# Performance work log

Hardware: AMD Instinct MI355X
Metric: run time of the kernel (lower is better)

Reference implementation:

```python
import jax, jax.numpy as jnp
import numpy as np

NEG_SLOPE = 0.2
CHUNK = 64  # target-node chunk size to bound the [B,c,N,H,D] intermediate


def layer_norm(x, g, b, eps=1e-5):
    mu = jnp.mean(x, axis=-1, keepdims=True)
    var = jnp.mean((x - mu) ** 2, axis=-1, keepdims=True)
    return (x - mu) / jnp.sqrt(var + eps) * g + b


def gatv2_dense(x, Wl, bl, Wr, br, att, bias):
    """GATv2 (PyG semantics, concat=True) on a fully-connected graph with self-loops.
    x: [B,N,Fin]; att: [H,D]. Returns [B,N,H*D].
    e_ij = att_h . leaky_relu(xl_j + xr_i); softmax over sources j; out_i = sum_j a_ij xl_j.
    """
    B, N, _ = x.shape
    H, D = att.shape
    xl = (x @ Wl + bl).reshape(B, N, H, D)  # source-side (lin_l)
    xr = (x @ Wr + br).reshape(B, N, H, D)  # target-side (lin_r)
    nc = N // CHUNK
    xr_ch = jnp.moveaxis(xr.reshape(B, nc, CHUNK, H, D), 1, 0)  # [nc,B,c,H,D]

    @jax.checkpoint
    def per_chunk(xr_c):  # xr_c: [B,c,H,D]
        z = jax.nn.leaky_relu(xr_c[:, :, None] + xl[:, None], NEG_SLOPE)  # [B,c,N,H,D]
        e = jnp.einsum('bcjhd,hd->bcjh', z, att)
        a = jax.nn.softmax(e, axis=2)  # softmax over sources j
        return jnp.einsum('bcjh,bjhd->bchd', a, xl)

    out = jax.lax.map(per_chunk, xr_ch)  # [nc,B,c,H,D]
    return jnp.moveaxis(out, 0, 1).reshape(B, N, H * D) + bias


def setup_inputs() -> dict:
    key = jax.random.key(0)
    ks = jax.random.split(key, 12)
    B, N, Fin, Hd, H, Do = 4, 2048, 32, 32, 4, 32
    f32 = jnp.float32

    def glorot(k, shape, fan_in):
        return jax.random.normal(k, shape, f32) * (1.0 / np.sqrt(fan_in))

    return {
        'x': jax.random.normal(ks[0], (B, N, Fin), f32),
        'embedding': jax.random.normal(ks[1], (N, Hd), f32),
        # layer 1: in=Fin, heads=H, head dim=Hd
        'Wl1': glorot(ks[2], (Fin, H * Hd), Fin), 'bl1': jnp.zeros((H * Hd,), f32),
        'Wr1': glorot(ks[3], (Fin, H * Hd), Fin), 'br1': jnp.zeros((H * Hd,), f32),
        'att1': glorot(ks[4], (H, Hd), Hd), 'bias1': jnp.zeros((H * Hd,), f32),
        'ln1_g': jnp.ones((H * Hd,), f32), 'ln1_b': jnp.zeros((H * Hd,), f32),
        # layer 2: in=H*Hd, heads=H, head dim=Do
        'Wl2': glorot(ks[5], (H * Hd, H * Do), H * Hd), 'bl2': jnp.zeros((H * Do,), f32),
        'Wr2': glorot(ks[6], (H * Hd, H * Do), H * Hd), 'br2': jnp.zeros((H * Do,), f32),
        'att2': glorot(ks[7], (H, Do), Do), 'bias2': jnp.zeros((H * Do,), f32),
        'ln2_g': jnp.ones((H * Do,), f32), 'ln2_b': jnp.zeros((H * Do,), f32),
    }


def reference(x, embedding, Wl1, bl1, Wr1, br1, att1, bias1, ln1_g, ln1_b,
              Wl2, bl2, Wr2, br2, att2, bias2, ln2_g, ln2_b):
    # AdaptiveAdjacency: cosine-similarity gram matrix. Its values are generically
    # all nonzero, so adj[b].nonzero() yields a fully-connected edge list including
    # self-loops; only the connectivity (dense) is consumed downstream.
    ne = embedding / jnp.linalg.norm(embedding, axis=1, keepdims=True)
    adj = ne @ ne.T  # [N,N]; connectivity only (dense), values unused by GATv2
    del adj

    h = layer_norm(gatv2_dense(x, Wl1, bl1, Wr1, br1, att1, bias1), ln1_g, ln1_b)
    h = jax.nn.relu(h)
    # dropout(p=0.3) is identity in eval mode
    out = layer_norm(gatv2_dense(h, Wl2, bl2, Wr2, br2, att2, bias2), ln2_g, ln2_b)
    return out
```

## Files before the change

### kernel.cpp

```cpp
#include <hip/hip_runtime.h>
#include <math.h>

#define LOG2E 1.4426950408889634f

constexpr int B_ = 4, N_ = 2048, H_ = 4, D_ = 32, HD_ = 128;
constexpr int BH_ = B_ * H_;
constexpr int ROWS_ = BH_ * N_;
constexpr size_t M_ = (size_t)ROWS_ * D_;

typedef float v2f __attribute__((ext_vector_type(2)));
typedef float v4f __attribute__((ext_vector_type(4)));
typedef _Float16 h2 __attribute__((ext_vector_type(2)));

static __device__ __forceinline__ void pkfma(v2f& o, v2f a, v2f b) {
    asm("v_pk_fma_f32 %0, %1, %2, %0" : "+v"(o) : "v"(a), "v"(b));
}
static __device__ __forceinline__ h2 habs2(h2 z) {
    unsigned int t = __builtin_bit_cast(unsigned int, z) & 0x7FFF7FFFu;
    return __builtin_bit_cast(h2, t);
}
static __device__ __forceinline__ h2 hadd2(unsigned int a, unsigned int b) {
    return __builtin_bit_cast(h2, a) + __builtin_bit_cast(h2, b);
}

__global__ __launch_bounds__(256) void k_linear(
    const float* __restrict__ x,
    const float* __restrict__ Wl, const float* __restrict__ bl,
    const float* __restrict__ Wr, const float* __restrict__ br,
    float* __restrict__ xl, unsigned short* __restrict__ xlh,
    unsigned short* __restrict__ xrh, int K)
{
    __shared__ __align__(16) float xs[32 * 128];
    const int tid = threadIdx.x;
    const int r0 = blockIdx.x * 32;
    const float4* src = (const float4*)(x + (size_t)r0 * K);
    float4* dst = (float4*)xs;
    for (int idx = tid; idx < 8 * K; idx += 256) dst[idx] = src[idx];
    __syncthreads();

    const int c  = tid & 127;
    const int rg = tid >> 7;
    float accl[16], accr[16];
    const float blv = bl[c], brv = br[c];
    #pragma unroll
    for (int r = 0; r < 16; r++) { accl[r] = blv; accr[r] = brv; }
    #pragma unroll 8
    for (int k = 0; k < K; k++) {
        const float wl = Wl[k * HD_ + c];
        const float wr = Wr[k * HD_ + c];
        #pragma unroll
        for (int r = 0; r < 16; r++) {
            const float xv = xs[(rg * 16 + r) * K + k];
            accl[r] = fmaf(xv, wl, accl[r]);
            accr[r] = fmaf(xv, wr, accr[r]);
        }
    }
    const int h = c >> 5, d = c & 31;
    #pragma unroll
    for (int r = 0; r < 16; r++) {
        const int row = r0 + rg * 16 + r;
        const int b = row >> 11, n = row & (N_ - 1);
        const size_t o = (((size_t)(b * H_ + h)) * N_ + n) * D_ + d;
        xl[o] = accl[r];
        xlh[o] = __builtin_bit_cast(unsigned short, (_Float16)accl[r]);
        xrh[o] = __builtin_bit_cast(unsigned short, (_Float16)accr[r]);
    }
}

__global__ __launch_bounds__(256) void k_u(
    const float* __restrict__ xl, const float* __restrict__ att,
    float* __restrict__ u)
{
    const int idx = blockIdx.x * 256 + threadIdx.x;
    const int h = (idx / N_) & (H_ - 1);
    const float4* a4 = (const float4*)(att + h * D_);
    const float4* l4 = (const float4*)(xl + (size_t)idx * D_);
    float su = 0.f;
    #pragma unroll
    for (int q = 0; q < 8; q++) {
        const float4 a = a4[q], lv = l4[q];
        su += a.x * lv.x + a.y * lv.y + a.z * lv.z + a.w * lv.w;
    }
    u[idx] = 0.6f * LOG2E * su;
}

__global__ __launch_bounds__(256) void k_attn(
    const float* __restrict__ xl, const unsigned int* __restrict__ xlh,
    const unsigned int* __restrict__ xrh,
    const float* __restrict__ u, const float* __restrict__ att,
    float* __restrict__ P, float* __restrict__ mb, float* __restrict__ lb,
    int jlen)
{
    __shared__ __align__(16) float xs[64 * D_];
    __shared__ __align__(16) unsigned int xh[64 * 16];
    __shared__ float us[64];
    const int tid = threadIdx.x, lane = tid & 63, wid = tid >> 6;
    const int blk = blockIdx.x & 127, part = blockIdx.x >> 7;
    const int bh = blk >> 3;
    const int i  = (blk & 7) * 256 + wid * 64 + lane;
    const int h  = bh & (H_ - 1);
    const int row = bh * N_ + i;

    h2 tc[16];
    {
        const float* ah = att + h * D_;
        #pragma unroll
        for (int q = 0; q < 16; q++) {
            h2 t;
            t.x = (_Float16)(ah[2 * q]     * (0.4f * LOG2E));
            t.y = (_Float16)(ah[2 * q + 1] * (0.4f * LOG2E));
            tc[q] = t;
        }
    }
    unsigned int xrp[16];
    {
        const uint4* s = (const uint4*)(xrh + (size_t)row * 16);
        const uint4 a = s[0], b = s[1], c = s[2], d = s[3];
        xrp[0]=a.x; xrp[1]=a.y; xrp[2]=a.z; xrp[3]=a.w;
        xrp[4]=b.x; xrp[5]=b.y; xrp[6]=b.z; xrp[7]=b.w;
        xrp[8]=c.x; xrp[9]=c.y; xrp[10]=c.z; xrp[11]=c.w;
        xrp[12]=d.x; xrp[13]=d.y; xrp[14]=d.z; xrp[15]=d.w;
    }

    float m = -INFINITY, l = 0.f;
    v2f o2[16];
    #pragma unroll
    for (int k = 0; k < 16; k++) o2[k] = (v2f){0.f, 0.f};

    const int jbeg = part * jlen, jend = jbeg + jlen;
    for (int j0 = jbeg; j0 < jend; j0 += 64) {
        const float4* s4 = (const float4*)(xl + ((size_t)bh * N_ + j0) * D_);
        ((float4*)xs)[tid] = s4[tid];
        ((float4*)xs)[tid + 256] = s4[tid + 256];
        const uint4* h4 = (const uint4*)(xlh + ((size_t)bh * N_ + j0) * 16);
        ((uint4*)xh)[tid] = h4[tid];
        if (tid < 64) us[tid] = u[bh * N_ + j0 + tid];
        __syncthreads();

        #pragma unroll 2
        for (int q = 0; q < 64; q++) {
            const uint4* hq = (const uint4*)(xh + q * 16);
            const uint4 w0 = hq[0], w1 = hq[1], w2 = hq[2], w3 = hq[3];
            float a0 = us[q], a1 = 0.f, a2 = 0.f, a3 = 0.f;
            a0 = __builtin_amdgcn_fdot2(habs2(hadd2(w0.x, xrp[0])),  tc[0],  a0, false);
            a1 = __builtin_amdgcn_fdot2(habs2(hadd2(w0.y, xrp[1])),  tc[1],  a1, false);
            a2 = __builtin_amdgcn_fdot2(habs2(hadd2(w0.z, xrp[2])),  tc[2],  a2, false);
            a3 = __builtin_amdgcn_fdot2(habs2(hadd2(w0.w, xrp[3])),  tc[3],  a3, false);
            a0 = __builtin_amdgcn_fdot2(habs2(hadd2(w1.x, xrp[4])),  tc[4],  a0, false);
            a1 = __builtin_amdgcn_fdot2(habs2(hadd2(w1.y, xrp[5])),  tc[5],  a1, false);
            a2 = __builtin_amdgcn_fdot2(habs2(hadd2(w1.z, xrp[6])),  tc[6],  a2, false);
            a3 = __builtin_amdgcn_fdot2(habs2(hadd2(w1.w, xrp[7])),  tc[7],  a3, false);
            a0 = __builtin_amdgcn_fdot2(habs2(hadd2(w2.x, xrp[8])),  tc[8],  a0, false);
            a1 = __builtin_amdgcn_fdot2(habs2(hadd2(w2.y, xrp[9])),  tc[9],  a1, false);
            a2 = __builtin_amdgcn_fdot2(habs2(hadd2(w2.z, xrp[10])), tc[10], a2, false);
            a3 = __builtin_amdgcn_fdot2(habs2(hadd2(w2.w, xrp[11])), tc[11], a3, false);
            a0 = __builtin_amdgcn_fdot2(habs2(hadd2(w3.x, xrp[12])), tc[12], a0, false);
            a1 = __builtin_amdgcn_fdot2(habs2(hadd2(w3.y, xrp[13])), tc[13], a1, false);
            a2 = __builtin_amdgcn_fdot2(habs2(hadd2(w3.z, xrp[14])), tc[14], a2, false);
            a3 = __builtin_amdgcn_fdot2(habs2(hadd2(w3.w, xrp[15])), tc[15], a3, false);
            const float e = (a0 + a1) + (a2 + a3);
            if (__builtin_expect(e > m, 0)) {
                const float al = exp2f(m - e);
                m = e;
                l *= al;
                const v2f alv = (v2f){al, al};
                #pragma unroll
                for (int k = 0; k < 16; k++) o2[k] *= alv;
            }
            const float p = exp2f(e - m);
            l += p;
            const v2f pp = (v2f){p, p};
            const v4f* rf = (const v4f*)(xs + q * D_);
            #pragma unroll
            for (int k = 0; k < 8; k++) {
                const v4f t = rf[k];
                pkfma(o2[2 * k],     pp, t.xy);
                pkfma(o2[2 * k + 1], pp, t.zw);
            }
        }
        __syncthreads();
    }

    float* Pp = P + (size_t)part * M_ + (size_t)row * D_;
    #pragma unroll
    for (int k = 0; k < 8; k++) {
        v4f w;
        w.xy = o2[2 * k]; w.zw = o2[2 * k + 1];
        ((v4f*)Pp)[k] = w;
    }
    mb[part * ROWS_ + row] = m;
    lb[part * ROWS_ + row] = l;
}

template <int JS>
__global__ __launch_bounds__(256) void k_combine(
    const float* __restrict__ P, const float* __restrict__ mb,
    const float* __restrict__ lb, float* __restrict__ ao)
{
    const int idx = blockIdx.x * 256 + threadIdx.x;
    const int row = idx >> 5;
    float mv[JS], lv[JS];
    #pragma unroll
    for (int s = 0; s < JS; s++) { mv[s] = mb[s * ROWS_ + row]; lv[s] = lb[s * ROWS_ + row]; }
    float M = mv[0];
    #pragma unroll
    for (int s = 1; s < JS; s++) M = fmaxf(M, mv[s]);
    float w[JS], L = 0.f;
    #pragma unroll
    for (int s = 0; s < JS; s++) { w[s] = exp2f(mv[s] - M); L += w[s] * lv[s]; }
    const float inv = 1.f / L;
    float acc = 0.f;
    #pragma unroll
    for (int s = 0; s < JS; s++) acc += w[s] * P[(size_t)s * M_ + idx];
    ao[idx] = acc * inv;
}

__global__ __launch_bounds__(64) void k_ln(
    const float* __restrict__ ain, const float* __restrict__ bias,
    const float* __restrict__ g, const float* __restrict__ bta,
    float* __restrict__ outp, int do_relu)
{
    const int row = blockIdx.x;
    const int b = row >> 11, n = row & (N_ - 1);
    const int t = threadIdx.x;
    const int c0 = t, c1 = t + 64;
    const size_t i0 = (((size_t)(b * H_ + (c0 >> 5))) * N_ + n) * D_ + (c0 & 31);
    const size_t i1 = (((size_t)(b * H_ + (c1 >> 5))) * N_ + n) * D_ + (c1 & 31);
    const float x0 = ain[i0] + bias[c0];
    const float x1 = ain[i1] + bias[c1];
    float s = x0 + x1;
    #pragma unroll
    for (int w = 1; w < 64; w <<= 1) s += __shfl_xor(s, w);
    const float mu = s * (1.f / 128.f);
    const float d0 = x0 - mu, d1 = x1 - mu;
    float q = d0 * d0 + d1 * d1;
    #pragma unroll
    for (int w = 1; w < 64; w <<= 1) q += __shfl_xor(q, w);
    const float rstd = rsqrtf(q * (1.f / 128.f) + 1e-5f);
    float y0 = d0 * rstd * g[c0] + bta[c0];
    float y1 = d1 * rstd * g[c1] + bta[c1];
    if (do_relu) { y0 = fmaxf(y0, 0.f); y1 = fmaxf(y1, 0.f); }
    outp[(size_t)row * HD_ + c0] = y0;
    outp[(size_t)row * HD_ + c1] = y1;
}

extern "C" void kernel_launch(void* const* d_in, const int* in_sizes, int n_in,
                              void* d_out, int out_size, void* d_ws, size_t ws_size,
                              hipStream_t stream) {
    const float* x    = (const float*)d_in[0];
    const float* Wl1  = (const float*)d_in[2];
    const float* bl1  = (const float*)d_in[3];
    const float* Wr1  = (const float*)d_in[4];
    const float* br1  = (const float*)d_in[5];
    const float* att1 = (const float*)d_in[6];
    const float* bias1= (const float*)d_in[7];
    const float* ln1g = (const float*)d_in[8];
    const float* ln1b = (const float*)d_in[9];
    const float* Wl2  = (const float*)d_in[10];
    const float* bl2  = (const float*)d_in[11];
    const float* Wr2  = (const float*)d_in[12];
    const float* br2  = (const float*)d_in[13];
    const float* att2 = (const float*)d_in[14];
    const float* bias2= (const float*)d_in[15];
    const float* ln2g = (const float*)d_in[16];
    const float* ln2b = (const float*)d_in[17];

    float* ws = (float*)d_ws;
    float* xl = ws;
    unsigned short* xlh = (unsigned short*)(xl + M_);
    unsigned short* xrh = xlh + M_;
    float* u  = xl + 2 * M_;

    int js = 1;
    for (int cand = 8; cand >= 1; cand >>= 1) {
        const size_t need = (2 * M_ + ROWS_ + (size_t)cand * (M_ + 2 * (size_t)ROWS_)) * sizeof(float);
        if (ws_size >= need) { js = cand; break; }
    }
    const int jlen = N_ / js;

    float* P  = u + ROWS_;
    float* mb = P + (size_t)js * M_;
    float* lb = mb + (size_t)js * ROWS_;
    float* h  = P;
    float* ao = xl;
    float* outf = (float*)d_out;

    const int BN = B_ * N_;
    k_linear<<<BN / 32, 256, 0, stream>>>(x, Wl1, bl1, Wr1, br1, xl, xlh, xrh, 32);
    k_u<<<ROWS_ / 256, 256, 0, stream>>>(xl, att1, u);
    k_attn<<<128 * js, 256, 0, stream>>>(xl, (const unsigned int*)xlh, (const unsigned int*)xrh,
                                         u, att1, P, mb, lb, jlen);
    if      (js == 8) k_combine<8><<<(ROWS_ * D_) / 256, 256, 0, stream>>>(P, mb, lb, ao);
    else if (js == 4) k_combine<4><<<(ROWS_ * D_) / 256, 256, 0, stream>>>(P, mb, lb, ao);
    else if (js == 2) k_combine<2><<<(ROWS_ * D_) / 256, 256, 0, stream>>>(P, mb, lb, ao);
    else              k_combine<1><<<(ROWS_ * D_) / 256, 256, 0, stream>>>(P, mb, lb, ao);
    k_ln<<<BN, 64, 0, stream>>>(ao, bias1, ln1g, ln1b, h, 1);
    k_linear<<<BN / 32, 256, 0, stream>>>(h, Wl2, bl2, Wr2, br2, xl, xlh, xrh, 128);
    k_u<<<ROWS_ / 256, 256, 0, stream>>>(xl, att2, u);
    k_attn<<<128 * js, 256, 0, stream>>>(xl, (const unsigned int*)xlh, (const unsigned int*)xrh,
                                         u, att2, P, mb, lb, jlen);
    if      (js == 8) k_combine<8><<<(ROWS_ * D_) / 256, 256, 0, stream>>>(P, mb, lb, ao);
    else if (js == 4) k_combine<4><<<(ROWS_ * D_) / 256, 256, 0, stream>>>(P, mb, lb, ao);
    else if (js == 2) k_combine<2><<<(ROWS_ * D_) / 256, 256, 0, stream>>>(P, mb, lb, ao);
    else              k_combine<1><<<(ROWS_ * D_) / 256, 256, 0, stream>>>(P, mb, lb, ao);
    k_ln<<<BN, 64, 0, stream>>>(ao, bias2, ln2g, ln2b, outf, 0);
}
```

Before: 451.7 us.

## Replace online softmax max-tracking with precomputed per-row upper bound

Adds a k_bound kernel that computes a per-target upper bound on the attention logit from max|xl| per channel, |xr| and max u. With that bound the attention loop can skip running-max rescaling, and the combine step becomes a plain sum of partials. k_attn drops shared-memory staging and block barriers in favour of 64-thread blocks reading source rows directly from global/cache, and the split count rises to 16. The cost is an extra small kernel, and a loose bound could make exp2 underflow and lose precision.

Result: slower. 631.6 us (+39.8%).

```diff
diff --git a/kernel.cpp b/kernel.cpp
--- a/kernel.cpp
+++ b/kernel.cpp
@@ -2,6 +2,12 @@
 #include <math.h>
 
 #define LOG2E 1.4426950408889634f
+
+#if __has_builtin(__builtin_amdgcn_exp2f)
+#define EXP2(x) __builtin_amdgcn_exp2f(x)
+#else
+#define EXP2(x) exp2f(x)
+#endif
 
 constexpr int B_ = 4, N_ = 2048, H_ = 4, D_ = 32, HD_ = 128;
 constexpr int BH_ = B_ * H_;
@@ -84,34 +90,84 @@
     u[idx] = 0.6f * LOG2E * su;
 }
 
-__global__ __launch_bounds__(256) void k_attn(
-    const float* __restrict__ xl, const unsigned int* __restrict__ xlh,
-    const unsigned int* __restrict__ xrh,
+__global__ __launch_bounds__(512) void k_bound(
+    const unsigned int* __restrict__ xlh, const unsigned int* __restrict__ xrh,
     const float* __restrict__ u, const float* __restrict__ att,
-    float* __restrict__ P, float* __restrict__ mb, float* __restrict__ lb,
-    int jlen)
-{
-    __shared__ __align__(16) float xs[64 * D_];
-    __shared__ __align__(16) unsigned int xh[64 * 16];
-    __shared__ float us[64];
-    const int tid = threadIdx.x, lane = tid & 63, wid = tid >> 6;
-    const int blk = blockIdx.x & 127, part = blockIdx.x >> 7;
-    const int bh = blk >> 3;
-    const int i  = (blk & 7) * 256 + wid * 64 + lane;
+    float* __restrict__ bound, unsigned int* __restrict__ tch)
+{
+    __shared__ float redA[16][33];
+    __shared__ float redB[16][33];
+    __shared__ float clv[32];
+    __shared__ float tca[32];
+    __shared__ float redu[512];
+    const int bh = blockIdx.x, h = bh & (H_ - 1), t = threadIdx.x;
+
+    if (bh < H_ && t < 16) {
+        h2 v;
+        v.x = (_Float16)(att[bh * D_ + 2 * t]     * (0.4f * LOG2E));
+        v.y = (_Float16)(att[bh * D_ + 2 * t + 1] * (0.4f * LOG2E));
+        tch[bh * 16 + t] = __builtin_bit_cast(unsigned int, v);
+    }
+    if (t < 16) {
+        _Float16 a = (_Float16)(att[h * D_ + 2 * t]     * (0.4f * LOG2E));
+        _Float16 b = (_Float16)(att[h * D_ + 2 * t + 1] * (0.4f * LOG2E));
+        tca[2 * t]     = fabsf((float)a);
+        tca[2 * t + 1] = fabsf((float)b);
+    }
+    const unsigned int* xb = xlh + (size_t)bh * N_ * 16;
+    const int p = t & 15, rg = t >> 4;
+    float m0 = 0.f, m1 = 0.f;
+    for (int r = rg; r < N_; r += 32) {
+        h2 z = __builtin_bit_cast(h2, xb[r * 16 + p] & 0x7FFF7FFFu);
+        m0 = fmaxf(m0, (float)z.x);
+        m1 = fmaxf(m1, (float)z.y);
+    }
+    redA[p][rg] = m0; redB[p][rg] = m1;
+    const float* ub = u + (size_t)bh * N_;
+    float um = -1e30f;
+    for (int r = t; r < N_; r += 512) um = fmaxf(um, ub[r]);
+    redu[t] = um;
+    __syncthreads();
+    if (t < 16) {
+        float a = 0.f, b = 0.f;
+        for (int g = 0; g < 32; g++) { a = fmaxf(a, redA[t][g]); b = fmaxf(b, redB[t][g]); }
+        clv[2 * t] = a; clv[2 * t + 1] = b;
+    }
+    for (int s = 256; s > 0; s >>= 1) {
+        if (t < s) redu[t] = fmaxf(redu[t], redu[t + s]);
+        __syncthreads();
+    }
+    const float umax = redu[0];
+    const unsigned int* xrb = xrh + (size_t)bh * N_ * 16;
+    for (int r = t; r < N_; r += 512) {
+        float s = 0.f;
+        #pragma unroll
+        for (int k = 0; k < 16; k++) {
+            h2 z = __builtin_bit_cast(h2, xrb[r * 16 + k] & 0x7FFF7FFFu);
+            s += tca[2 * k] * (clv[2 * k] + (float)z.x)
+               + tca[2 * k + 1] * (clv[2 * k + 1] + (float)z.y);
+        }
+        bound[bh * N_ + r] = umax + s + 0.25f;
+    }
+}
+
+__global__ __launch_bounds__(64) void k_attn(
+    const float* __restrict__ xlf, const unsigned int* __restrict__ xlh,
+    const unsigned int* __restrict__ xrh, const float* __restrict__ u,
+    const float* __restrict__ bound, const unsigned int* __restrict__ tch,
+    float* __restrict__ P, float* __restrict__ lb, int jlen)
+{
+    const int lane = threadIdx.x;
+    const int part = blockIdx.x >> 9;
+    const int t512 = blockIdx.x & 511;
+    const int bh = t512 >> 5;
     const int h  = bh & (H_ - 1);
-    const int row = bh * N_ + i;
+    const int row = bh * N_ + (t512 & 31) * 64 + lane;
 
     h2 tc[16];
-    {
-        const float* ah = att + h * D_;
-        #pragma unroll
-        for (int q = 0; q < 16; q++) {
-            h2 t;
-            t.x = (_Float16)(ah[2 * q]     * (0.4f * LOG2E));
-            t.y = (_Float16)(ah[2 * q + 1] * (0.4f * LOG2E));
-            tc[q] = t;
-        }
-    }
+    #pragma unroll
+    for (int k = 0; k < 16; k++) tc[k] = __builtin_bit_cast(h2, tch[h * 16 + k]);
+
     unsigned int xrp[16];
     {
         const uint4* s = (const uint4*)(xrh + (size_t)row * 16);
@@ -121,64 +177,49 @@
         xrp[8]=c.x; xrp[9]=c.y; xrp[10]=c.z; xrp[11]=c.w;
         xrp[12]=d.x; xrp[13]=d.y; xrp[14]=d.z; xrp[15]=d.w;
     }
-
-    float m = -INFINITY, l = 0.f;
+    const float negb = -bound[row];
+
+    float l0 = 0.f, l1 = 0.f;
     v2f o2[16];
     #pragma unroll
     for (int k = 0; k < 16; k++) o2[k] = (v2f){0.f, 0.f};
 
+    const unsigned int* xlh_b = xlh + (size_t)bh * N_ * 16;
+    const float* u_b  = u + (size_t)bh * N_;
+    const float* xl_b = xlf + (size_t)bh * N_ * D_;
+
     const int jbeg = part * jlen, jend = jbeg + jlen;
-    for (int j0 = jbeg; j0 < jend; j0 += 64) {
-        const float4* s4 = (const float4*)(xl + ((size_t)bh * N_ + j0) * D_);
-        ((float4*)xs)[tid] = s4[tid];
-        ((float4*)xs)[tid + 256] = s4[tid + 256];
-        const uint4* h4 = (const uint4*)(xlh + ((size_t)bh * N_ + j0) * 16);
-        ((uint4*)xh)[tid] = h4[tid];
-        if (tid < 64) us[tid] = u[bh * N_ + j0 + tid];
-        __syncthreads();
-
-        #pragma unroll 2
-        for (int q = 0; q < 64; q++) {
-            const uint4* hq = (const uint4*)(xh + q * 16);
-            const uint4 w0 = hq[0], w1 = hq[1], w2 = hq[2], w3 = hq[3];
-            float a0 = us[q], a1 = 0.f, a2 = 0.f, a3 = 0.f;
-            a0 = __builtin_amdgcn_fdot2(habs2(hadd2(w0.x, xrp[0])),  tc[0],  a0, false);
-            a1 = __builtin_amdgcn_fdot2(habs2(hadd2(w0.y, xrp[1])),  tc[1],  a1, false);
-            a2 = __builtin_amdgcn_fdot2(habs2(hadd2(w0.z, xrp[2])),  tc[2],  a2, false);
-            a3 = __builtin_amdgcn_fdot2(habs2(hadd2(w0.w, xrp[3])),  tc[3],  a3, false);
-            a0 = __builtin_amdgcn_fdot2(habs2(hadd2(w1.x, xrp[4])),  tc[4],  a0, false);
-            a1 = __builtin_amdgcn_fdot2(habs2(hadd2(w1.y, xrp[5])),  tc[5],  a1, false);
-            a2 = __builtin_amdgcn_fdot2(habs2(hadd2(w1.z, xrp[6])),  tc[6],  a2, false);
-            a3 = __builtin_amdgcn_fdot2(habs2(hadd2(w1.w, xrp[7])),  tc[7],  a3, false);
-            a0 = __builtin_amdgcn_fdot2(habs2(hadd2(w2.x, xrp[8])),  tc[8],  a0, false);
-            a1 = __builtin_amdgcn_fdot2(habs2(hadd2(w2.y, xrp[9])),  tc[9],  a1, false);
-            a2 = __builtin_amdgcn_fdot2(habs2(hadd2(w2.z, xrp[10])), tc[10], a2, false);
-            a3 = __builtin_amdgcn_fdot2(habs2(hadd2(w2.w, xrp[11])), tc[11], a3, false);
-            a0 = __builtin_amdgcn_fdot2(habs2(hadd2(w3.x, xrp[12])), tc[12], a0, false);
-            a1 = __builtin_amdgcn_fdot2(habs2(hadd2(w3.y, xrp[13])), tc[13], a1, false);
-            a2 = __builtin_amdgcn_fdot2(habs2(hadd2(w3.z, xrp[14])), tc[14], a2, false);
-            a3 = __builtin_amdgcn_fdot2(habs2(hadd2(w3.w, xrp[15])), tc[15], a3, false);
-            const float e = (a0 + a1) + (a2 + a3);
-            if (__builtin_expect(e > m, 0)) {
-                const float al = exp2f(m - e);
-                m = e;
-                l *= al;
-                const v2f alv = (v2f){al, al};
-                #pragma unroll
-                for (int k = 0; k < 16; k++) o2[k] *= alv;
-            }
-            const float p = exp2f(e - m);
-            l += p;
-            const v2f pp = (v2f){p, p};
-            const v4f* rf = (const v4f*)(xs + q * D_);
-            #pragma unroll
-            for (int k = 0; k < 8; k++) {
-                const v4f t = rf[k];
-                pkfma(o2[2 * k],     pp, t.xy);
-                pkfma(o2[2 * k + 1], pp, t.zw);
-            }
+    #pragma unroll 2
+    for (int j = jbeg; j < jend; j++) {
+        const uint4* hq = (const uint4*)(xlh_b + (size_t)j * 16);
+        const uint4 w0 = hq[0], w1 = hq[1], w2 = hq[2], w3 = hq[3];
+        float a0 = u_b[j] + negb, a1 = 0.f, a2 = 0.f, a3 = 0.f;
+        a0 = __builtin_amdgcn_fdot2(habs2(hadd2(w0.x, xrp[0])),  tc[0],  a0, false);
+        a1 = __builtin_amdgcn_fdot2(habs2(hadd2(w0.y, xrp[1])),  tc[1],  a1, false);
+        a2 = __builtin_amdgcn_fdot2(habs2(hadd2(w0.z, xrp[2])),  tc[2],  a2, false);
+        a3 = __builtin_amdgcn_fdot2(habs2(hadd2(w0.w, xrp[3])),  tc[3],  a3, false);
+        a0 = __builtin_amdgcn_fdot2(habs2(hadd2(w1.x, xrp[4])),  tc[4],  a0, false);
+        a1 = __builtin_amdgcn_fdot2(habs2(hadd2(w1.y, xrp[5])),  tc[5],  a1, false);
+        a2 = __builtin_amdgcn_fdot2(habs2(hadd2(w1.z, xrp[6])),  tc[6],  a2, false);
+        a3 = __builtin_amdgcn_fdot2(habs2(hadd2(w1.w, xrp[7])),  tc[7],  a3, false);
+        a0 = __builtin_amdgcn_fdot2(habs2(hadd2(w2.x, xrp[8])),  tc[8],  a0, false);
+        a1 = __builtin_amdgcn_fdot2(habs2(hadd2(w2.y, xrp[9])),  tc[9],  a1, false);
+        a2 = __builtin_amdgcn_fdot2(habs2(hadd2(w2.z, xrp[10])), tc[10], a2, false);
+        a3 = __builtin_amdgcn_fdot2(habs2(hadd2(w2.w, xrp[11])), tc[11], a3, false);
+        a0 = __builtin_amdgcn_fdot2(habs2(hadd2(w3.x, xrp[12])), tc[12], a0, false);
+        a1 = __builtin_amdgcn_fdot2(habs2(hadd2(w3.y, xrp[13])), tc[13], a1, false);
+        a2 = __builtin_amdgcn_fdot2(habs2(hadd2(w3.z, xrp[14])), tc[14], a2, false);
+        a3 = __builtin_amdgcn_fdot2(habs2(hadd2(w3.w, xrp[15])), tc[15], a3, false);
+        const float p = EXP2((a0 + a1) + (a2 + a3));
+        if (j & 1) l1 += p; else l0 += p;
+        v2f pp; pp.x = p; pp.y = p;
+        const v4f* rf = (const v4f*)(xl_b + (size_t)j * D_);
+        #pragma unroll
+        for (int k2 = 0; k2 < 8; k2++) {
+            const v4f t = rf[k2];
+            pkfma(o2[2 * k2],     pp, t.xy);
+            pkfma(o2[2 * k2 + 1], pp, t.zw);
         }
-        __syncthreads();
     }
 
     float* Pp = P + (size_t)part * M_ + (size_t)row * D_;
@@ -188,31 +229,23 @@
         w.xy = o2[2 * k]; w.zw = o2[2 * k + 1];
         ((v4f*)Pp)[k] = w;
     }
-    mb[part * ROWS_ + row] = m;
-    lb[part * ROWS_ + row] = l;
+    lb[part * ROWS_ + row] = l0 + l1;
 }
 
 template <int JS>
 __global__ __launch_bounds__(256) void k_combine(
-    const float* __restrict__ P, const float* __restrict__ mb,
-    const float* __restrict__ lb, float* __restrict__ ao)
+    const float* __restrict__ P, const float* __restrict__ lb,
+    float* __restrict__ ao)
 {
     const int idx = blockIdx.x * 256 + threadIdx.x;
     const int row = idx >> 5;
-    float mv[JS], lv[JS];
-    #pragma unroll
-    for (int s = 0; s < JS; s++) { mv[s] = mb[s * ROWS_ + row]; lv[s] = lb[s * ROWS_ + row]; }
-    float M = mv[0];
-    #pragma unroll
-    for (int s = 1; s < JS; s++) M = fmaxf(M, mv[s]);
-    float w[JS], L = 0.f;
-    #pragma unroll
-    for (int s = 0; s < JS; s++) { w[s] = exp2f(mv[s] - M); L += w[s] * lv[s]; }
-    const float inv = 1.f / L;
+    float L = 0.f;
+    #pragma unroll
+    for (int s = 0; s < JS; s++) L += lb[s * ROWS_ + row];
     float acc = 0.f;
     #pragma unroll
-    for (int s = 0; s < JS; s++) acc += w[s] * P[(size_t)s * M_ + idx];
-    ao[idx] = acc * inv;
+    for (int s = 0; s < JS; s++) acc += P[(size_t)s * M_ + idx];
+    ao[idx] = acc / L;
 }
 
 __global__ __launch_bounds__(64) void k_ln(
@@ -269,18 +302,20 @@
     float* xl = ws;
     unsigned short* xlh = (unsigned short*)(xl + M_);
     unsigned short* xrh = xlh + M_;
-    float* u  = xl + 2 * M_;
+    float* u     = xl + 2 * M_;
+    float* bound = u + ROWS_;
+    unsigned int* tch = (unsigned int*)(bound + ROWS_);
 
     int js = 1;
-    for (int cand = 8; cand >= 1; cand >>= 1) {
-        const size_t need = (2 * M_ + ROWS_ + (size_t)cand * (M_ + 2 * (size_t)ROWS_)) * sizeof(float);
+    for (int cand = 16; cand >= 1; cand >>= 1) {
+        const size_t need = ((size_t)2 * M_ + 2 * ROWS_ + 64
+                             + (size_t)cand * (M_ + ROWS_)) * sizeof(float);
         if (ws_size >= need) { js = cand; break; }
     }
     const int jlen = N_ / js;
 
-    float* P  = u + ROWS_;
-    float* mb = P + (size_t)js * M_;
-    float* lb = mb + (size_t)js * ROWS_;
+    float* P  = (float*)(tch + 64);
+    float* lb = P + (size_t)js * M_;
     float* h  = P;
     float* ao = xl;
     float* outf = (float*)d_out;
@@ -288,20 +323,26 @@
     const int BN = B_ * N_;
     k_linear<<<BN / 32, 256, 0, stream>>>(x, Wl1, bl1, Wr1, br1, xl, xlh, xrh, 32);
     k_u<<<ROWS_ / 256, 256, 0, stream>>>(xl, att1, u);
-    k_attn<<<128 * js, 256, 0, stream>>>(xl, (const unsigned int*)xlh, (const unsigned int*)xrh,
-                                         u, att1, P, mb, lb, jlen);
-    if      (js == 8) k_combine<8><<<(ROWS_ * D_) / 256, 256, 0, stream>>>(P, mb, lb, ao);
-    else if (js == 4) k_combine<4><<<(ROWS_ * D_) / 256, 256, 0, stream>>>(P, mb, lb, ao);
-    else if (js == 2) k_combine<2><<<(ROWS_ * D_) / 256, 256, 0, stream>>>(P, mb, lb, ao);
-    else              k_combine<1><<<(ROWS_ * D_) / 256, 256, 0, stream>>>(P, mb, lb, ao);
+    k_bound<<<BH_, 512, 0, stream>>>((const unsigned int*)xlh, (const unsigned int*)xrh,
+                                     u, att1, bound, tch);
+    k_attn<<<512 * js, 64, 0, stream>>>(xl, (const unsigned int*)xlh, (const unsigned int*)xrh,
+                                        u, bound, tch, P, lb, jlen);
+    if      (js == 16) k_combine<16><<<(ROWS_ * D_) / 256, 256, 0, stream>>>(P, lb, ao);
+    else if (js == 8)  k_combine<8><<<(ROWS_ * D_) / 256, 256, 0, stream>>>(P, lb, ao);
+    else if (js == 4)  k_combine<4><<<(ROWS_ * D_) / 256, 256, 0, stream>>>(P, lb, ao);
+    else if (js == 2)  k_combine<2><<<(ROWS_ * D_) / 256, 256, 0, stream>>>(P, lb, ao);
+    else               k_combine<1><<<(ROWS_ * D_) / 256, 256, 0, stream>>>(P, lb, ao);
     k_ln<<<BN, 64, 0, stream>>>(ao, bias1, ln1g, ln1b, h, 1);
     k_linear<<<BN / 32, 256, 0, stream>>>(h, Wl2, bl2, Wr2, br2, xl, xlh, xrh, 128);
     k_u<<<ROWS_ / 256, 256, 0, stream>>>(xl, att2, u);
-    k_attn<<<128 * js, 256, 0, stream>>>(xl, (const unsigned int*)xlh, (const unsigned int*)xrh,
-                                         u, att2, P, mb, lb, jlen);
-    if      (js == 8) k_combine<8><<<(ROWS_ * D_) / 256, 256, 0, stream>>>(P, mb, lb, ao);
-    else if (js == 4) k_combine<4><<<(ROWS_ * D_) / 256, 256, 0, stream>>>(P, mb, lb, ao);
-    else if (js == 2) k_combine<2><<<(ROWS_ * D_) / 256, 256, 0, stream>>>(P, mb, lb, ao);
-    else              k_combine<1><<<(ROWS_ * D_) / 256, 256, 0, stream>>>(P, mb, lb, ao);
+    k_bound<<<BH_, 512, 0, stream>>>((const unsigned int*)xlh, (const unsigned int*)xrh,
+                                     u, att2, bound, tch);
+    k_attn<<<512 * js, 64, 0, stream>>>(xl, (const unsigned int*)xlh, (const unsigned int*)xrh,
+                                        u, bound, tch, P, lb, jlen);
+    if      (js == 16) k_combine<16><<<(ROWS_ * D_) / 256, 256, 0, stream>>>(P, lb, ao);
+    else if (js == 8)  k_combine<8><<<(ROWS_ * D_) / 256, 256, 0, stream>>>(P, lb, ao);
+    else if (js == 4)  k_combine<4><<<(ROWS_ * D_) / 256, 256, 0, stream>>>(P, lb, ao);
+    else if (js == 2)  k_combine<2><<<(ROWS_ * D_) / 256, 256, 0, stream>>>(P, lb, ao);
+    else               k_combine<1><<<(ROWS_ * D_) / 256, 256, 0, stream>>>(P, lb, ao);
     k_ln<<<BN, 64, 0, stream>>>(ao, bias2, ln2g, ln2b, outf, 0);
 }
```
